# Kernel tuning notes

Hardware: AMD Instinct MI355X
Metric: run time of the kernel (lower is better)

## Reference

```python
import jax, jax.numpy as jnp
import numpy as np

B, S, MEM, D, H = 4, 1024, 1024, 1024, 16
T = S + MEM          # total_len (memory + current segment)
DK = D // H          # 64


def setup_inputs() -> dict:
    key = jax.random.key(0)
    ks = jax.random.split(key, 12)
    wscale = 1.0 / np.sqrt(D).astype(np.float32)
    q = jax.random.normal(ks[0], (B, S, D), jnp.float32)
    k = jax.random.normal(ks[1], (B, T, D), jnp.float32)
    v = jax.random.normal(ks[2], (B, T, D), jnp.float32)
    u = jax.random.normal(ks[3], (1, H, 1, DK), jnp.float32)
    v_bias = jax.random.normal(ks[4], (1, H, 1, DK), jnp.float32)
    Wq = jax.random.normal(ks[5], (D, D), jnp.float32) * wscale
    Wk = jax.random.normal(ks[6], (D, D), jnp.float32) * wscale
    Wv = jax.random.normal(ks[7], (D, D), jnp.float32) * wscale
    Wr = jax.random.normal(ks[8], (D, D), jnp.float32) * wscale
    Wo = jax.random.normal(ks[9], (D, D), jnp.float32) * wscale
    R = jax.random.normal(ks[10], (T, D), jnp.float32)  # positional encodings
    # TXL causal mask: query i may attend to keys j <= i + MEM
    causal = jnp.tril(jnp.ones((S, T), jnp.bool_), k=MEM)
    mask = jnp.broadcast_to(causal[None], (B, S, T))
    return {"q": q, "k": k, "v": v, "mask": mask, "u": u, "v_bias": v_bias,
            "Wq": Wq, "Wk": Wk, "Wv": Wv, "Wr": Wr, "Wo": Wo, "R": R}


def circulant_shift(x, shift):
    # Matches torch: gather cols with idx[i, j] = (roll(arange(W), shift)[j] + i) % W
    h, w = x.shape[-2], x.shape[-1]
    idx = (jnp.roll(jnp.arange(w), shift)[None, :] + jnp.arange(h)[:, None]) % w
    return jnp.take_along_axis(x, idx[None, None], axis=-1)


def reference(q, k, v, mask, u, v_bias, Wq, Wk, Wv, Wr, Wo, R):
    # projections (nn.Linear: y = x @ W.T), split heads -> [B, H, L, DK]
    qh = (q @ Wq.T).reshape(B, S, H, DK).transpose(0, 2, 1, 3)
    kh = (k @ Wk.T).reshape(B, T, H, DK).transpose(0, 2, 1, 3)
    vh = (v @ Wv.T).reshape(B, T, H, DK).transpose(0, 2, 1, 3)
    rh = (R[-T:] @ Wr.T).reshape(1, T, H, DK).transpose(0, 2, 1, 3)
    ac = jnp.einsum('bhid,bhjd->bhij', qh + u, kh)         # content term
    bd = jnp.einsum('bhid,bhjd->bhij', qh + v_bias, rh)    # position term
    bd = circulant_shift(bd, -S + 1)
    score = (ac + bd) / np.sqrt(DK).astype(np.float32)
    score = jnp.where(mask[:, None], score, -jnp.inf)      # mask==0 -> -inf
    att = jax.nn.softmax(score, axis=-1)                   # dropout p=0
    o = jnp.einsum('bhij,bhjd->bhid', att, vh)             # [B, H, S, DK]
    concat = o.transpose(0, 2, 1, 3).reshape(B, S, D)
    return concat @ Wo.T
```

## Files before the change

kernel.cpp:

```cpp
#include <hip/hip_runtime.h>
#include <hip/hip_bf16.h>
#include <stdint.h>

#define Ss   1024
#define MEMm 1024
#define Tt   2048
#define Dd   1024
#define Hh   16
#define DKk  64

typedef unsigned short u16;
using f32x4 = __attribute__((ext_vector_type(4))) float;
using s16x8 = __attribute__((ext_vector_type(8))) short;

__device__ __forceinline__ u16 f2bf(float x) {
  __hip_bfloat16 h = __float2bfloat16(x);
  return *(reinterpret_cast<u16*>(&h));
}
__device__ __forceinline__ float b2f(short s) {
  union { uint32_t u; float f; } c; c.u = ((uint32_t)(u16)s) << 16; return c.f;
}
__device__ __forceinline__ uint32_t pk2(float lo, float hi) {
  return (uint32_t)f2bf(lo) | ((uint32_t)f2bf(hi) << 16);
}
__device__ __forceinline__ f32x4 mfma16(s16x8 a, s16x8 b, f32x4 c) {
  return __builtin_amdgcn_mfma_f32_16x16x32_bf16(a, b, c, 0, 0, 0);
}
__device__ __forceinline__ void gl_lds16(const u16* g, u16* l) {
  __builtin_amdgcn_global_load_lds(
      (const __attribute__((address_space(1))) uint32_t*)g,
      (__attribute__((address_space(3))) uint32_t*)l, 16, 0, 0);
}

__global__ __launch_bounds__(256)
void cvt5(const float* __restrict__ w0, const float* __restrict__ w1,
          const float* __restrict__ w2, const float* __restrict__ w3,
          const float* __restrict__ w4, u16* __restrict__ dst) {
  const float* s;
  switch (blockIdx.y) {
    case 0: s = w0; break; case 1: s = w1; break; case 2: s = w2; break;
    case 3: s = w3; break; default: s = w4; break;
  }
  const int idx = blockIdx.x * 256 + threadIdx.x;
  const float4* p = (const float4*)(s + (size_t)idx * 8);
  const float4 a = p[0], bq = p[1];
  uint4 o;
  o.x = pk2(a.x, a.y);   o.y = pk2(a.z, a.w);
  o.z = pk2(bq.x, bq.y); o.w = pk2(bq.z, bq.w);
  *(uint4*)(dst + ((size_t)blockIdx.y << 20) + (size_t)idx * 8) = o;
}

__global__ __launch_bounds__(256)
void cvt2(const float* __restrict__ s0, u16* __restrict__ d0, int n80,
          const float* __restrict__ s1, u16* __restrict__ d1, int n81) {
  const float* s = blockIdx.y ? s1 : s0;
  u16* d = blockIdx.y ? d1 : d0;
  const int n8 = blockIdx.y ? n81 : n80;
  int i = blockIdx.x * 256 + threadIdx.x;
  const int stride = gridDim.x * 256;
  for (; i < n8; i += stride) {
    const float4* p = (const float4*)(s + (size_t)i * 8);
    const float4 a = p[0], bq = p[1];
    uint4 o;
    o.x = pk2(a.x, a.y);   o.y = pk2(a.z, a.w);
    o.z = pk2(bq.x, bq.y); o.w = pk2(bq.z, bq.w);
    *(uint4*)(d + (size_t)i * 8) = o;
  }
}

template <int EPI>
__device__ __forceinline__
void gemm_body(const u16* __restrict__ X, const u16* __restrict__ W,
               void* __restrict__ O, int n0, int m0, u16* As, u16* Bs) {
  const int tid = threadIdx.x;
  const int lane = tid & 63, wave = tid >> 6;
  const int fr = lane & 15, fq = lane >> 4;
  const int wr = (wave >> 1) * 64, wc = (wave & 1) * 64;
  f32x4 acc[4][4] = {};

  const int lrow = lane >> 2, lcol = (lane & 3) * 8;
  const u16* xg0 = X + (size_t)(n0 + wave * 16 + lrow) * Dd + lcol;
  const u16* xg1 = X + (size_t)(n0 + 64 + wave * 16 + lrow) * Dd + lcol;
  const u16* wg0 = W + (size_t)(m0 + wave * 16 + lrow) * Dd + lcol;
  const u16* wg1 = W + (size_t)(m0 + 64 + wave * 16 + lrow) * Dd + lcol;
  u16* la0 = &As[(wave * 16) * 32];
  u16* la1 = &As[(64 + wave * 16) * 32];
  u16* lb0 = &Bs[(wave * 16) * 32];
  u16* lb1 = &Bs[(64 + wave * 16) * 32];

  for (int k0 = 0; k0 < Dd; k0 += 32) {
    gl_lds16(xg0 + k0, la0);
    gl_lds16(xg1 + k0, la1);
    gl_lds16(wg0 + k0, lb0);
    gl_lds16(wg1 + k0, lb1);
    __syncthreads();
    s16x8 af[4], bfv[4];
#pragma unroll
    for (int i = 0; i < 4; ++i)
      af[i] = *(const s16x8*)&As[(wr + i * 16 + fr) * 32 + fq * 8];
#pragma unroll
    for (int j = 0; j < 4; ++j)
      bfv[j] = *(const s16x8*)&Bs[(wc + j * 16 + fr) * 32 + fq * 8];
#pragma unroll
    for (int i = 0; i < 4; ++i)
#pragma unroll
      for (int j = 0; j < 4; ++j)
        acc[i][j] = mfma16(af[i], bfv[j], acc[i][j]);
    __syncthreads();
  }

#pragma unroll
  for (int i = 0; i < 4; ++i)
#pragma unroll
    for (int j = 0; j < 4; ++j) {
      if constexpr (EPI == 2) {
        const int grow = n0 + wr + i * 16 + fq * 4;
        const int m = m0 + wc + j * 16 + fr;
        const int bb = grow >> 11, t = grow & 2047;
        const int hh = m >> 6, dk = m & 63;
        ushort4 pk4;
        pk4.x = f2bf(acc[i][j][0]); pk4.y = f2bf(acc[i][j][1]);
        pk4.z = f2bf(acc[i][j][2]); pk4.w = f2bf(acc[i][j][3]);
        *(ushort4*)&((u16*)O)[(((size_t)(bb * Hh + hh) * DKk + dk) << 11) + t] = pk4;
      } else {
#pragma unroll
        for (int r = 0; r < 4; ++r) {
          const int n = n0 + wr + i * 16 + fq * 4 + r;
          const int m = m0 + wc + j * 16 + fr;
          const float y = acc[i][j][r];
          if constexpr (EPI == 0) {
            const int bb = n >> 10, s = n & 1023, hh = m >> 6, dk = m & 63;
            ((u16*)O)[((size_t)(bb * Hh + hh) * Ss + s) * DKk + dk] = f2bf(y);
          } else if constexpr (EPI == 1) {
            const int bb = n >> 11, t = n & 2047, hh = m >> 6, dk = m & 63;
            ((u16*)O)[((size_t)(bb * Hh + hh) * Tt + t) * DKk + dk] = f2bf(y);
          } else if constexpr (EPI == 3) {
            const int hh = m >> 6, dk = m & 63;
            ((u16*)O)[((size_t)hh * Tt + n) * DKk + dk] = f2bf(y);
          } else {
            ((float*)O)[(size_t)n * Dd + m] = y;
          }
        }
      }
    }
}

__global__ __launch_bounds__(256)
void gemm_kv(const u16* __restrict__ ACT, const u16* __restrict__ Wb,
             u16* __restrict__ KH, u16* __restrict__ VT) {
  __shared__ u16 As[128 * 32];
  __shared__ u16 Bs[128 * 32];
  const int bid = blockIdx.x;
  const int isV = bid >= 512;
  const int t = bid & 511;
  const int n0 = (t >> 3) * 128, m0 = (t & 7) * 128;
  const u16* X = ACT + (isV ? ((size_t)8 << 20) : 0);
  const u16* W = Wb + ((size_t)(isV ? 2 : 1) << 20);
  if (isV) gemm_body<2>(X, W, VT, n0, m0, As, Bs);
  else     gemm_body<1>(X, W, KH, n0, m0, As, Bs);
}

__global__ __launch_bounds__(256)
void gemm_qr(const u16* __restrict__ ACT, const u16* __restrict__ Wb,
             u16* __restrict__ QH, u16* __restrict__ RH) {
  __shared__ u16 As[128 * 32];
  __shared__ u16 Bs[128 * 32];
  const int bid = blockIdx.x;
  const int isR = bid >= 256;
  const int t = isR ? (bid - 256) : bid;
  const int n0 = (t >> 3) * 128, m0 = (t & 7) * 128;
  const u16* X = ACT + (isR ? ((size_t)4 << 20) : 0);
  const u16* W = Wb + ((size_t)(isR ? 3 : 0) << 20);
  if (isR) gemm_body<3>(X, W, RH, n0, m0, As, Bs);
  else     gemm_body<0>(X, W, QH, n0, m0, As, Bs);
}

__global__ __launch_bounds__(256)
void gemm_o(const u16* __restrict__ X, const u16* __restrict__ W,
            float* __restrict__ O) {
  __shared__ u16 As[128 * 32];
  __shared__ u16 Bs[128 * 32];
  gemm_body<4>(X, W, O, blockIdx.x * 128, blockIdx.y * 128, As, Bs);
}

__global__ __launch_bounds__(256, 2)
void attn7(const u16* __restrict__ QH, const u16* __restrict__ KH,
           const u16* __restrict__ VT, const u16* __restrict__ RH,
           const float* __restrict__ ub, const float* __restrict__ vbb,
           u16* __restrict__ CONCAT) {
  __shared__ u16 Ks[64 * 64];
  __shared__ u16 Vt[64 * 64];
  __shared__ u16 RB[256 * 64];
  __shared__ u16 Pl[4][2][16 * 72];

  const int tid = threadIdx.x;
  const int wave = tid >> 6, lane = tid & 63;
  const int fr = lane & 15, fq = lane >> 4;

  const int wid = blockIdx.x;
  const int bx = (wid < 256) ? (wid >> 6) : (11 - (wid >> 6));
  const int bh = wid & 63;
  const int h = bh & 15, b = bh >> 4;
  const int i0 = bx * 128;
  const int r0 = i0 + wave * 32;
  const int nch = 2 * bx + 18;
  const int base = (i0 + 1023) & 2047;

  const u16* qB  = QH + (size_t)bh * (Ss * DKk);
  const u16* khB = KH + (size_t)bh * (Tt * DKk);
  const u16* vtB = VT + (size_t)bh * (DKk * Tt);
  const u16* rhB = RH + (size_t)h * (Tt * DKk);

  float ulo[8], uhi[8], vlo[8], vhi[8];
  {
    const float* up = ub + h * 64 + fq * 8;
    const float* vp = vbb + h * 64 + fq * 8;
    *(float4*)&ulo[0] = *(const float4*)up;
    *(float4*)&ulo[4] = *(const float4*)(up + 4);
    *(float4*)&uhi[0] = *(const float4*)(up + 32);
    *(float4*)&uhi[4] = *(const float4*)(up + 36);
    *(float4*)&vlo[0] = *(const float4*)vp;
    *(float4*)&vlo[4] = *(const float4*)(vp + 4);
    *(float4*)&vhi[0] = *(const float4*)(vp + 32);
    *(float4*)&vhi[4] = *(const float4*)(vp + 36);
  }

  s16x8 qu[2][2], qv[2][2];
#pragma unroll
  for (int s = 0; s < 2; ++s) {
    const u16* qp = qB + (size_t)(r0 + s * 16 + fr) * DKk + fq * 8;
    const s16x8 q0 = *(const s16x8*)qp;
    const s16x8 q1 = *(const s16x8*)(qp + 32);
    union U8 { s16x8 v; uint32_t w[4]; } a0, a1, c0, c1;
#pragma unroll
    for (int e = 0; e < 4; ++e) {
      a0.w[e] = pk2(b2f(q0[2*e]) + ulo[2*e], b2f(q0[2*e+1]) + ulo[2*e+1]);
      a1.w[e] = pk2(b2f(q1[2*e]) + uhi[2*e], b2f(q1[2*e+1]) + uhi[2*e+1]);
      c0.w[e] = pk2(b2f(q0[2*e]) + vlo[2*e], b2f(q0[2*e+1]) + vlo[2*e+1]);
      c1.w[e] = pk2(b2f(q1[2*e]) + vhi[2*e], b2f(q1[2*e+1]) + vhi[2*e+1]);
    }
    qu[s][0] = a0.v; qu[s][1] = a1.v; qv[s][0] = c0.v; qv[s][1] = c1.v;
  }

  s16x8 vone;
  {
    union U8 { s16x8 v; uint32_t w[4]; } o;
    const uint32_t f = (fr == 0) ? 0x3F803F80u : 0u;
#pragma unroll
    for (int e = 0; e < 4; ++e) o.w[e] = f;
    vone = o.v;
  }

  const int srow = lane >> 3, sch = lane & 7;
  const int row0 = wave * 8 + srow;
  const int row1 = wave * 8 + 32 + srow;
  const int swc = (sch ^ srow) * 8;

#pragma unroll
  for (int p = 0; p < 6; ++p) {
    const int off = p * 32 + wave * 8 + srow;
    const uint4 rr =
        *(const uint4*)(rhB + (size_t)((base + off) & 2047) * 64 + swc);
    *(uint4*)&RB[off * 64 + sch * 8] = rr;
  }
  {
    const uint4 k0 = *(const uint4*)(khB + (size_t)row0 * 64 + swc);
    const uint4 k1 = *(const uint4*)(khB + (size_t)row1 * 64 + swc);
    const uint4 v0 = *(const uint4*)(vtB + (size_t)row0 * Tt + swc);
    const uint4 v1 = *(const uint4*)(vtB + (size_t)row1 * Tt + swc);
    *(uint4*)&Ks[row0 * 64 + sch * 8] = k0;
    *(uint4*)&Ks[row1 * 64 + sch * 8] = k1;
    *(uint4*)&Vt[row0 * 64 + sch * 8] = v0;
    *(uint4*)&Vt[row1 * 64 + sch * 8] = v1;
  }

  f32x4 oacc[2][4] = {};
  f32x4 oacc2[2] = {};
  float mrun[2][4];
#pragma unroll
  for (int s = 0; s < 2; ++s)
#pragma unroll
    for (int r = 0; r < 4; ++r) mrun[s][r] = -1e30f;

  const float SC = 0.18033688011f;

  for (int c = 0; c < nch; ++c) {
    const int j0 = c * 64;
    const bool more = (c + 1 < nch);
    __syncthreads();

    uint4 kr0, kr1, vr0, vr1;
    if (more) {
      kr0 = *(const uint4*)(khB + (size_t)(j0 + 64 + row0) * 64 + swc);
      kr1 = *(const uint4*)(khB + (size_t)(j0 + 64 + row1) * 64 + swc);
      vr0 = *(const uint4*)(vtB + (size_t)row0 * Tt + (j0 + 64) + swc);
      vr1 = *(const uint4*)(vtB + (size_t)row1 * Tt + (j0 + 64) + swc);
    }
    const int offA0 = j0 + 192 + wave * 8 + srow;
    const int offA1 = offA0 + 32;
    const uint4 rr0 =
        *(const uint4*)(rhB + (size_t)((base + offA0) & 2047) * 64 + swc);
    const uint4 rr1 =
        *(const uint4*)(rhB + (size_t)((base + offA1) & 2047) * 64 + swc);

    s16x8 rf[6][2];
#pragma unroll
    for (int mt = 0; mt < 6; ++mt) {
      const int rho = (j0 + wave * 32 + mt * 16 + fr) & 255;
#pragma unroll
      for (int hh = 0; hh < 2; ++hh)
        rf[mt][hh] = *(const s16x8*)&RB[rho * 64 + (((hh * 4 + fq) ^ (rho & 7)) * 8)];
    }

    f32x4 g[2][5];
    __builtin_amdgcn_s_setprio(1);
#pragma unroll
    for (int s = 0; s < 2; ++s)
#pragma unroll
      for (int k = 0; k < 5; ++k) {
        f32x4 t = {};
        t = mfma16(qv[s][0], rf[s + k][0], t);
        t = mfma16(qv[s][1], rf[s + k][1], t);
        g[s][k] = t;
      }
    __builtin_amdgcn_s_setprio(0);

    s16x8 kf[4][2];
#pragma unroll
    for (int ct = 0; ct < 4; ++ct) {
      const int row = ct * 16 + fr;
#pragma unroll
      for (int hh = 0; hh < 2; ++hh)
        kf[ct][hh] = *(const s16x8*)&Ks[row * 64 + (((hh * 4 + fq) ^ (row & 7)) * 8)];
    }

    f32x4 pacc[2][4];
#pragma unroll
    for (int s = 0; s < 2; ++s) {
#pragma unroll
      for (int r = 0; r < 4; ++r) {
        const int sum = fq * 4 + r + fr;
        const int src = fq * 16 + (sum & 15);
        const bool cy = sum >= 16;
        const float s0 = __shfl(g[s][0][r], src);
        const float s1 = __shfl(g[s][1][r], src);
        const float s2 = __shfl(g[s][2][r], src);
        const float s3 = __shfl(g[s][3][r], src);
        const float s4 = __shfl(g[s][4][r], src);
        pacc[s][0][r] = cy ? s1 : s0;
        pacc[s][1][r] = cy ? s2 : s1;
        pacc[s][2][r] = cy ? s3 : s2;
        pacc[s][3][r] = cy ? s4 : s3;
      }
    }
    __builtin_amdgcn_s_setprio(1);
#pragma unroll
    for (int s = 0; s < 2; ++s)
#pragma unroll
      for (int ct = 0; ct < 4; ++ct) {
        pacc[s][ct] = mfma16(qu[s][0], kf[ct][0], pacc[s][ct]);
        pacc[s][ct] = mfma16(qu[s][1], kf[ct][1], pacc[s][ct]);
      }
    __builtin_amdgcn_s_setprio(0);

#pragma unroll
    for (int s = 0; s < 2; ++s) {
      const int rbase = r0 + s * 16;
      if (j0 + 63 > rbase + MEMm) {
#pragma unroll
        for (int ct = 0; ct < 4; ++ct)
#pragma unroll
          for (int r = 0; r < 4; ++r) {
            const int gi = rbase + fq * 4 + r, gj = j0 + ct * 16 + fr;
            const float vv = pacc[s][ct][r] * SC;
            pacc[s][ct][r] = (gj > gi + MEMm) ? -1e30f : vv;
          }
      } else {
#pragma unroll
        for (int ct = 0; ct < 4; ++ct)
#pragma unroll
          for (int r = 0; r < 4; ++r) pacc[s][ct][r] *= SC;
      }
      float alpha[4];
#pragma unroll
      for (int r = 0; r < 4; ++r) {
        float cm = fmaxf(fmaxf(pacc[s][0][r], pacc[s][1][r]),
                         fmaxf(pacc[s][2][r], pacc[s][3][r]));
        int v = __builtin_bit_cast(int, cm);
        int t2 = __builtin_amdgcn_update_dpp(v, v, 0xB1, 0xF, 0xF, true);
        cm = fmaxf(cm, __builtin_bit_cast(float, t2)); v = __builtin_bit_cast(int, cm);
        t2 = __builtin_amdgcn_update_dpp(v, v, 0x4E, 0xF, 0xF, true);
        cm = fmaxf(cm, __builtin_bit_cast(float, t2)); v = __builtin_bit_cast(int, cm);
        t2 = __builtin_amdgcn_update_dpp(v, v, 0x141, 0xF, 0xF, true);
        cm = fmaxf(cm, __builtin_bit_cast(float, t2)); v = __builtin_bit_cast(int, cm);
        t2 = __builtin_amdgcn_update_dpp(v, v, 0x140, 0xF, 0xF, true);
        cm = fmaxf(cm, __builtin_bit_cast(float, t2));
        const float mn = fmaxf(mrun[s][r], cm);
        alpha[r] = exp2f(mrun[s][r] - mn);
        mrun[s][r] = mn;
      }
#pragma unroll
      for (int ct = 0; ct < 4; ++ct)
#pragma unroll
        for (int r = 0; r < 4; ++r)
          pacc[s][ct][r] = exp2f(pacc[s][ct][r] - mrun[s][r]);
#pragma unroll
      for (int t = 0; t < 4; ++t)
#pragma unroll
        for (int r = 0; r < 4; ++r) oacc[s][t][r] *= alpha[r];
#pragma unroll
      for (int r = 0; r < 4; ++r) oacc2[s][r] *= alpha[r];
    }

#pragma unroll
    for (int s = 0; s < 2; ++s)
#pragma unroll
      for (int ct = 0; ct < 4; ++ct)
#pragma unroll
        for (int r = 0; r < 4; ++r)
          Pl[wave][s][(fq * 4 + r) * 72 + ct * 16 + fr] = f2bf(pacc[s][ct][r]);
    asm volatile("s_waitcnt lgkmcnt(0)" ::: "memory");
    __builtin_amdgcn_sched_barrier(0);
    s16x8 ap[2][2];
#pragma unroll
    for (int s = 0; s < 2; ++s)
#pragma unroll
      for (int hh = 0; hh < 2; ++hh)
        ap[s][hh] = *(const s16x8*)&Pl[wave][s][fr * 72 + hh * 32 + fq * 8];

    s16x8 vf[4][2];
#pragma unroll
    for (int nt = 0; nt < 4; ++nt) {
      const int row = nt * 16 + fr;
#pragma unroll
      for (int hh = 0; hh < 2; ++hh)
        vf[nt][hh] = *(const s16x8*)&Vt[row * 64 + (((hh * 4 + fq) ^ (row & 7)) * 8)];
    }
    __builtin_amdgcn_s_setprio(1);
#pragma unroll
    for (int s = 0; s < 2; ++s) {
#pragma unroll
      for (int nt = 0; nt < 4; ++nt) {
        oacc[s][nt] = mfma16(ap[s][0], vf[nt][0], oacc[s][nt]);
        oacc[s][nt] = mfma16(ap[s][1], vf[nt][1], oacc[s][nt]);
      }
      oacc2[s] = mfma16(ap[s][0], vone, oacc2[s]);
      oacc2[s] = mfma16(ap[s][1], vone, oacc2[s]);
    }
    __builtin_amdgcn_s_setprio(0);

    __syncthreads();
    if (more) {
      *(uint4*)&Ks[row0 * 64 + sch * 8] = kr0;
      *(uint4*)&Ks[row1 * 64 + sch * 8] = kr1;
      *(uint4*)&Vt[row0 * 64 + sch * 8] = vr0;
      *(uint4*)&Vt[row1 * 64 + sch * 8] = vr1;
    }
    *(uint4*)&RB[(offA0 & 255) * 64 + sch * 8] = rr0;
    *(uint4*)&RB[(offA1 & 255) * 64 + sch * 8] = rr1;
  }

#pragma unroll
  for (int s = 0; s < 2; ++s) {
    float linv[4];
#pragma unroll
    for (int r = 0; r < 4; ++r)
      linv[r] = 1.0f / __shfl(oacc2[s][r], lane & 48);
#pragma unroll
    for (int nt = 0; nt < 4; ++nt)
#pragma unroll
      for (int r = 0; r < 4; ++r) {
        const int gi = r0 + s * 16 + fq * 4 + r;
        CONCAT[((size_t)b * Ss + gi) * Dd + h * DKk + nt * 16 + fr] =
            f2bf(oacc[s][nt][r] * linv[r]);
      }
  }
}

extern "C" void kernel_launch(void* const* d_in, const int* in_sizes, int n_in,
                              void* d_out, int out_size, void* d_ws,
                              size_t ws_size, hipStream_t stream) {
  (void)in_sizes; (void)n_in; (void)out_size; (void)ws_size;
  const float* q  = (const float*)d_in[0];
  const float* k  = (const float*)d_in[1];
  const float* v  = (const float*)d_in[2];
  const float* u  = (const float*)d_in[4];
  const float* vb = (const float*)d_in[5];
  const float* Wq = (const float*)d_in[6];
  const float* Wk = (const float*)d_in[7];
  const float* Wv = (const float*)d_in[8];
  const float* Wr = (const float*)d_in[9];
  const float* Wo = (const float*)d_in[10];
  const float* R  = (const float*)d_in[11];

  char* ws = (char*)d_ws;
  u16* QH  = (u16*)ws; ws += 8388608;
  u16* KH  = (u16*)ws; ws += 16777216;
  u16* VT  = (u16*)ws; ws += 16777216;
  u16* RH  = (u16*)ws; ws += 4194304;
  u16* Wb  = (u16*)ws; ws += 10485760;
  u16* STG = (u16*)ws;

  const size_t M1 = (size_t)1 << 20;

  cvt5<<<dim3(512, 5), 256, 0, stream>>>(Wq, Wk, Wv, Wr, Wo, Wb);
  cvt2<<<dim3(2048, 2), 256, 0, stream>>>(k, STG, 1048576,
                                          v, STG + ((size_t)8 << 20), 1048576);
  gemm_kv<<<1024, 256, 0, stream>>>(STG, Wb, KH, VT);
  cvt2<<<dim3(1024, 2), 256, 0, stream>>>(q, STG, 524288,
                                          R, STG + ((size_t)4 << 20), 262144);
  gemm_qr<<<384, 256, 0, stream>>>(STG, Wb, QH, RH);
  attn7<<<512, 256, 0, stream>>>(QH, KH, VT, RH, u, vb, STG);
  gemm_o<<<dim3(32, 8), 256, 0, stream>>>(STG, Wb + 4 * M1, (float*)d_out);
}
```

Measured before the change: 249.7 us.

## Merge conversion and projection launches, fuse fp32 q/R conversion, lazy softmax rescale

Folds the weight and k/v fp32-to-bf16 conversions into one launch, and folds all four projection GEMMs (Q, K, V, R) into a single launch. The Q and R GEMMs now read fp32 activations directly and convert them to bf16 in registers before writing to shared memory, which removes a separate conversion pass and the extra round trip through global memory. In attention, the running max and the output accumulators are only rescaled when some lane's chunk max exceeds the running max by a threshold, skipping most exp2 and multiply work. The lazy rescale lets exponents rise to about 2^11 above the stored max, which is safe in fp32 but may slightly change the bf16 rounding of P. The fp32 path also loads A through registers, giving up the async direct-to-LDS load.

New measurement: 241.6 us. 3.3% less time.

```diff
diff --git a/kernel.cpp b/kernel.cpp
--- a/kernel.cpp
+++ b/kernel.cpp
@@ -33,29 +33,23 @@
 }
 
 __global__ __launch_bounds__(256)
-void cvt5(const float* __restrict__ w0, const float* __restrict__ w1,
+void cvt7(const float* __restrict__ w0, const float* __restrict__ w1,
           const float* __restrict__ w2, const float* __restrict__ w3,
-          const float* __restrict__ w4, u16* __restrict__ dst) {
+          const float* __restrict__ w4, const float* __restrict__ kk,
+          const float* __restrict__ vv, u16* __restrict__ Wb,
+          u16* __restrict__ kd, u16* __restrict__ vd) {
   const float* s;
+  u16* d;
+  int n8;
   switch (blockIdx.y) {
-    case 0: s = w0; break; case 1: s = w1; break; case 2: s = w2; break;
-    case 3: s = w3; break; default: s = w4; break;
-  }
-  const int idx = blockIdx.x * 256 + threadIdx.x;
-  const float4* p = (const float4*)(s + (size_t)idx * 8);
-  const float4 a = p[0], bq = p[1];
-  uint4 o;
-  o.x = pk2(a.x, a.y);   o.y = pk2(a.z, a.w);
-  o.z = pk2(bq.x, bq.y); o.w = pk2(bq.z, bq.w);
-  *(uint4*)(dst + ((size_t)blockIdx.y << 20) + (size_t)idx * 8) = o;
-}
-
-__global__ __launch_bounds__(256)
-void cvt2(const float* __restrict__ s0, u16* __restrict__ d0, int n80,
-          const float* __restrict__ s1, u16* __restrict__ d1, int n81) {
-  const float* s = blockIdx.y ? s1 : s0;
-  u16* d = blockIdx.y ? d1 : d0;
-  const int n8 = blockIdx.y ? n81 : n80;
+    case 0: s = w0; d = Wb;                     n8 = 131072;  break;
+    case 1: s = w1; d = Wb + ((size_t)1 << 20); n8 = 131072;  break;
+    case 2: s = w2; d = Wb + ((size_t)2 << 20); n8 = 131072;  break;
+    case 3: s = w3; d = Wb + ((size_t)3 << 20); n8 = 131072;  break;
+    case 4: s = w4; d = Wb + ((size_t)4 << 20); n8 = 131072;  break;
+    case 5: s = kk; d = kd;                     n8 = 1048576; break;
+    default: s = vv; d = vd;                    n8 = 1048576; break;
+  }
   int i = blockIdx.x * 256 + threadIdx.x;
   const int stride = gridDim.x * 256;
   for (; i < n8; i += stride) {
@@ -70,45 +64,10 @@
 
 template <int EPI>
 __device__ __forceinline__
-void gemm_body(const u16* __restrict__ X, const u16* __restrict__ W,
-               void* __restrict__ O, int n0, int m0, u16* As, u16* Bs) {
-  const int tid = threadIdx.x;
-  const int lane = tid & 63, wave = tid >> 6;
+void gemm_epi(f32x4 (&acc)[4][4], void* __restrict__ O, int n0, int m0) {
+  const int lane = threadIdx.x & 63, wave = threadIdx.x >> 6;
   const int fr = lane & 15, fq = lane >> 4;
   const int wr = (wave >> 1) * 64, wc = (wave & 1) * 64;
-  f32x4 acc[4][4] = {};
-
-  const int lrow = lane >> 2, lcol = (lane & 3) * 8;
-  const u16* xg0 = X + (size_t)(n0 + wave * 16 + lrow) * Dd + lcol;
-  const u16* xg1 = X + (size_t)(n0 + 64 + wave * 16 + lrow) * Dd + lcol;
-  const u16* wg0 = W + (size_t)(m0 + wave * 16 + lrow) * Dd + lcol;
-  const u16* wg1 = W + (size_t)(m0 + 64 + wave * 16 + lrow) * Dd + lcol;
-  u16* la0 = &As[(wave * 16) * 32];
-  u16* la1 = &As[(64 + wave * 16) * 32];
-  u16* lb0 = &Bs[(wave * 16) * 32];
-  u16* lb1 = &Bs[(64 + wave * 16) * 32];
-
-  for (int k0 = 0; k0 < Dd; k0 += 32) {
-    gl_lds16(xg0 + k0, la0);
-    gl_lds16(xg1 + k0, la1);
-    gl_lds16(wg0 + k0, lb0);
-    gl_lds16(wg1 + k0, lb1);
-    __syncthreads();
-    s16x8 af[4], bfv[4];
-#pragma unroll
-    for (int i = 0; i < 4; ++i)
-      af[i] = *(const s16x8*)&As[(wr + i * 16 + fr) * 32 + fq * 8];
-#pragma unroll
-    for (int j = 0; j < 4; ++j)
-      bfv[j] = *(const s16x8*)&Bs[(wc + j * 16 + fr) * 32 + fq * 8];
-#pragma unroll
-    for (int i = 0; i < 4; ++i)
-#pragma unroll
-      for (int j = 0; j < 4; ++j)
-        acc[i][j] = mfma16(af[i], bfv[j], acc[i][j]);
-    __syncthreads();
-  }
-
 #pragma unroll
   for (int i = 0; i < 4; ++i)
 #pragma unroll
@@ -145,34 +104,126 @@
     }
 }
 
+template <int EPI>
+__device__ __forceinline__
+void gemm_body(const u16* __restrict__ X, const u16* __restrict__ W,
+               void* __restrict__ O, int n0, int m0, u16* As, u16* Bs) {
+  const int tid = threadIdx.x;
+  const int lane = tid & 63, wave = tid >> 6;
+  const int fr = lane & 15, fq = lane >> 4;
+  const int wr = (wave >> 1) * 64, wc = (wave & 1) * 64;
+  f32x4 acc[4][4] = {};
+
+  const int lrow = lane >> 2, lcol = (lane & 3) * 8;
+  const u16* xg0 = X + (size_t)(n0 + wave * 16 + lrow) * Dd + lcol;
+  const u16* xg1 = X + (size_t)(n0 + 64 + wave * 16 + lrow) * Dd + lcol;
+  const u16* wg0 = W + (size_t)(m0 + wave * 16 + lrow) * Dd + lcol;
+  const u16* wg1 = W + (size_t)(m0 + 64 + wave * 16 + lrow) * Dd + lcol;
+  u16* la0 = &As[(wave * 16) * 32];
+  u16* la1 = &As[(64 + wave * 16) * 32];
+  u16* lb0 = &Bs[(wave * 16) * 32];
+  u16* lb1 = &Bs[(64 + wave * 16) * 32];
+
+  for (int k0 = 0; k0 < Dd; k0 += 32) {
+    gl_lds16(xg0 + k0, la0);
+    gl_lds16(xg1 + k0, la1);
+    gl_lds16(wg0 + k0, lb0);
+    gl_lds16(wg1 + k0, lb1);
+    __syncthreads();
+    s16x8 af[4], bfv[4];
+#pragma unroll
+    for (int i = 0; i < 4; ++i)
+      af[i] = *(const s16x8*)&As[(wr + i * 16 + fr) * 32 + fq * 8];
+#pragma unroll
+    for (int j = 0; j < 4; ++j)
+      bfv[j] = *(const s16x8*)&Bs[(wc + j * 16 + fr) * 32 + fq * 8];
+#pragma unroll
+    for (int i = 0; i < 4; ++i)
+#pragma unroll
+      for (int j = 0; j < 4; ++j)
+        acc[i][j] = mfma16(af[i], bfv[j], acc[i][j]);
+    __syncthreads();
+  }
+  gemm_epi<EPI>(acc, O, n0, m0);
+}
+
+template <int EPI>
+__device__ __forceinline__
+void gemm_body_f32(const float* __restrict__ X, const u16* __restrict__ W,
+                   void* __restrict__ O, int n0, int m0, u16* As, u16* Bs) {
+  const int tid = threadIdx.x;
+  const int lane = tid & 63, wave = tid >> 6;
+  const int fr = lane & 15, fq = lane >> 4;
+  const int wr = (wave >> 1) * 64, wc = (wave & 1) * 64;
+  f32x4 acc[4][4] = {};
+
+  const int arow = tid >> 1, acol = (tid & 1) * 16;
+  const float* xg = X + (size_t)(n0 + arow) * Dd + acol;
+  u16* aw = &As[arow * 32 + acol];
+
+  const int lrow = lane >> 2, lcol = (lane & 3) * 8;
+  const u16* wg0 = W + (size_t)(m0 + wave * 16 + lrow) * Dd + lcol;
+  const u16* wg1 = W + (size_t)(m0 + 64 + wave * 16 + lrow) * Dd + lcol;
+  u16* lb0 = &Bs[(wave * 16) * 32];
+  u16* lb1 = &Bs[(64 + wave * 16) * 32];
+
+  for (int k0 = 0; k0 < Dd; k0 += 32) {
+    const float4 f0 = *(const float4*)(xg + k0);
+    const float4 f1 = *(const float4*)(xg + k0 + 4);
+    const float4 f2 = *(const float4*)(xg + k0 + 8);
+    const float4 f3 = *(const float4*)(xg + k0 + 12);
+    __syncthreads();
+    gl_lds16(wg0 + k0, lb0);
+    gl_lds16(wg1 + k0, lb1);
+    uint4 p0, p1;
+    p0.x = pk2(f0.x, f0.y); p0.y = pk2(f0.z, f0.w);
+    p0.z = pk2(f1.x, f1.y); p0.w = pk2(f1.z, f1.w);
+    p1.x = pk2(f2.x, f2.y); p1.y = pk2(f2.z, f2.w);
+    p1.z = pk2(f3.x, f3.y); p1.w = pk2(f3.z, f3.w);
+    *(uint4*)aw = p0;
+    *(uint4*)(aw + 8) = p1;
+    __syncthreads();
+    s16x8 af[4], bfv[4];
+#pragma unroll
+    for (int i = 0; i < 4; ++i)
+      af[i] = *(const s16x8*)&As[(wr + i * 16 + fr) * 32 + fq * 8];
+#pragma unroll
+    for (int j = 0; j < 4; ++j)
+      bfv[j] = *(const s16x8*)&Bs[(wc + j * 16 + fr) * 32 + fq * 8];
+#pragma unroll
+    for (int i = 0; i < 4; ++i)
+#pragma unroll
+      for (int j = 0; j < 4; ++j)
+        acc[i][j] = mfma16(af[i], bfv[j], acc[i][j]);
+  }
+  gemm_epi<EPI>(acc, O, n0, m0);
+}
+
 __global__ __launch_bounds__(256)
-void gemm_kv(const u16* __restrict__ ACT, const u16* __restrict__ Wb,
-             u16* __restrict__ KH, u16* __restrict__ VT) {
+void gemm_all(const u16* __restrict__ kstg, const u16* __restrict__ vstg,
+              const float* __restrict__ qf, const float* __restrict__ Rf,
+              const u16* __restrict__ Wb,
+              u16* __restrict__ QH, u16* __restrict__ KH,
+              u16* __restrict__ VT, u16* __restrict__ RH) {
   __shared__ u16 As[128 * 32];
   __shared__ u16 Bs[128 * 32];
   const int bid = blockIdx.x;
-  const int isV = bid >= 512;
-  const int t = bid & 511;
-  const int n0 = (t >> 3) * 128, m0 = (t & 7) * 128;
-  const u16* X = ACT + (isV ? ((size_t)8 << 20) : 0);
-  const u16* W = Wb + ((size_t)(isV ? 2 : 1) << 20);
-  if (isV) gemm_body<2>(X, W, VT, n0, m0, As, Bs);
-  else     gemm_body<1>(X, W, KH, n0, m0, As, Bs);
-}
-
-__global__ __launch_bounds__(256)
-void gemm_qr(const u16* __restrict__ ACT, const u16* __restrict__ Wb,
-             u16* __restrict__ QH, u16* __restrict__ RH) {
-  __shared__ u16 As[128 * 32];
-  __shared__ u16 Bs[128 * 32];
-  const int bid = blockIdx.x;
-  const int isR = bid >= 256;
-  const int t = isR ? (bid - 256) : bid;
-  const int n0 = (t >> 3) * 128, m0 = (t & 7) * 128;
-  const u16* X = ACT + (isR ? ((size_t)4 << 20) : 0);
-  const u16* W = Wb + ((size_t)(isR ? 3 : 0) << 20);
-  if (isR) gemm_body<3>(X, W, RH, n0, m0, As, Bs);
-  else     gemm_body<0>(X, W, QH, n0, m0, As, Bs);
+  if (bid < 512) {
+    const int t = bid;
+    gemm_body<1>(kstg, Wb + ((size_t)1 << 20), KH,
+                 (t >> 3) * 128, (t & 7) * 128, As, Bs);
+  } else if (bid < 1024) {
+    const int t = bid - 512;
+    gemm_body<2>(vstg, Wb + ((size_t)2 << 20), VT,
+                 (t >> 3) * 128, (t & 7) * 128, As, Bs);
+  } else if (bid < 1280) {
+    const int t = bid - 1024;
+    gemm_body_f32<0>(qf, Wb, QH, (t >> 3) * 128, (t & 7) * 128, As, Bs);
+  } else {
+    const int t = bid - 1280;
+    gemm_body_f32<3>(Rf, Wb + ((size_t)3 << 20), RH,
+                     (t >> 3) * 128, (t & 7) * 128, As, Bs);
+  }
 }
 
 __global__ __launch_bounds__(256)
@@ -180,6 +231,9 @@
             float* __restrict__ O) {
   __shared__ u16 As[128 * 32];
   __shared__ u16 Bs[128 * 32];
+  const int tid = threadIdx.x;
+  const int lane = tid & 63, wave = tid >> 6;
+  (void)lane; (void)wave;
   gemm_body<4>(X, W, O, blockIdx.x * 128, blockIdx.y * 128, As, Bs);
 }
 
@@ -283,6 +337,7 @@
     for (int r = 0; r < 4; ++r) mrun[s][r] = -1e30f;
 
   const float SC = 0.18033688011f;
+  const float THR = 11.0f;
 
   for (int c = 0; c < nch; ++c) {
     const int j0 = c * 64;
@@ -381,35 +436,45 @@
 #pragma unroll
           for (int r = 0; r < 4; ++r) pacc[s][ct][r] *= SC;
       }
-      float alpha[4];
+      float cm[4];
 #pragma unroll
       for (int r = 0; r < 4; ++r) {
-        float cm = fmaxf(fmaxf(pacc[s][0][r], pacc[s][1][r]),
-                         fmaxf(pacc[s][2][r], pacc[s][3][r]));
-        int v = __builtin_bit_cast(int, cm);
+        float t = fmaxf(fmaxf(pacc[s][0][r], pacc[s][1][r]),
+                        fmaxf(pacc[s][2][r], pacc[s][3][r]));
+        int v = __builtin_bit_cast(int, t);
         int t2 = __builtin_amdgcn_update_dpp(v, v, 0xB1, 0xF, 0xF, true);
-        cm = fmaxf(cm, __builtin_bit_cast(float, t2)); v = __builtin_bit_cast(int, cm);
+        t = fmaxf(t, __builtin_bit_cast(float, t2)); v = __builtin_bit_cast(int, t);
         t2 = __builtin_amdgcn_update_dpp(v, v, 0x4E, 0xF, 0xF, true);
-        cm = fmaxf(cm, __builtin_bit_cast(float, t2)); v = __builtin_bit_cast(int, cm);
+        t = fmaxf(t, __builtin_bit_cast(float, t2)); v = __builtin_bit_cast(int, t);
         t2 = __builtin_amdgcn_update_dpp(v, v, 0x141, 0xF, 0xF, true);
-        cm = fmaxf(cm, __builtin_bit_cast(float, t2)); v = __builtin_bit_cast(int, cm);
+        t = fmaxf(t, __builtin_bit_cast(float, t2)); v = __builtin_bit_cast(int, t);
         t2 = __builtin_amdgcn_update_dpp(v, v, 0x140, 0xF, 0xF, true);
-        cm = fmaxf(cm, __builtin_bit_cast(float, t2));
-        const float mn = fmaxf(mrun[s][r], cm);
-        alpha[r] = exp2f(mrun[s][r] - mn);
-        mrun[s][r] = mn;
+        t = fmaxf(t, __builtin_bit_cast(float, t2));
+        cm[r] = t;
+      }
+      bool need = false;
+#pragma unroll
+      for (int r = 0; r < 4; ++r) need = need || (cm[r] > mrun[s][r] + THR);
+      if (__any(need)) {
+        float alpha[4];
+#pragma unroll
+        for (int r = 0; r < 4; ++r) {
+          const float mn = fmaxf(mrun[s][r], cm[r]);
+          alpha[r] = exp2f(mrun[s][r] - mn);
+          mrun[s][r] = mn;
+        }
+#pragma unroll
+        for (int t = 0; t < 4; ++t)
+#pragma unroll
+          for (int r = 0; r < 4; ++r) oacc[s][t][r] *= alpha[r];
+#pragma unroll
+        for (int r = 0; r < 4; ++r) oacc2[s][r] *= alpha[r];
       }
 #pragma unroll
       for (int ct = 0; ct < 4; ++ct)
 #pragma unroll
         for (int r = 0; r < 4; ++r)
           pacc[s][ct][r] = exp2f(pacc[s][ct][r] - mrun[s][r]);
-#pragma unroll
-      for (int t = 0; t < 4; ++t)
-#pragma unroll
-        for (int r = 0; r < 4; ++r) oacc[s][t][r] *= alpha[r];
-#pragma unroll
-      for (int r = 0; r < 4; ++r) oacc2[s][r] *= alpha[r];
     }
 
 #pragma unroll
@@ -502,14 +567,12 @@
   u16* STG = (u16*)ws;
 
   const size_t M1 = (size_t)1 << 20;
-
-  cvt5<<<dim3(512, 5), 256, 0, stream>>>(Wq, Wk, Wv, Wr, Wo, Wb);
-  cvt2<<<dim3(2048, 2), 256, 0, stream>>>(k, STG, 1048576,
-                                          v, STG + ((size_t)8 << 20), 1048576);
-  gemm_kv<<<1024, 256, 0, stream>>>(STG, Wb, KH, VT);
-  cvt2<<<dim3(1024, 2), 256, 0, stream>>>(q, STG, 524288,
-                                          R, STG + ((size_t)4 << 20), 262144);
-  gemm_qr<<<384, 256, 0, stream>>>(STG, Wb, QH, RH);
+  u16* kstg = STG;
+  u16* vstg = STG + ((size_t)8 << 20);
+
+  cvt7<<<dim3(512, 7), 256, 0, stream>>>(Wq, Wk, Wv, Wr, Wo, k, v,
+                                         Wb, kstg, vstg);
+  gemm_all<<<1408, 256, 0, stream>>>(kstg, vstg, q, R, Wb, QH, KH, VT, RH);
   attn7<<<512, 256, 0, stream>>>(QH, KH, VT, RH, u, vb, STG);
   gemm_o<<<dim3(32, 8), 256, 0, stream>>>(STG, Wb + 4 * M1, (float*)d_out);
 }
```
